# Performance work log

Hardware: AMD Instinct MI355X
Metric: run time of the kernel (lower is better)

Reference implementation:

```python
import jax, jax.numpy as jnp
import numpy as np

B, L, H, W = 16, 4096, 64, 64
SEQ = 1024  # target_sequence_length (hardcoded in the torch module)
SP = 32     # sqrt(SEQ)


def _conv1d(x, w, b, pad):
    y = jax.lax.conv_general_dilated(x, w, (1,), [(pad, pad)],
                                     dimension_numbers=('NCH', 'OIH', 'NCH'))
    return y + b[None, :, None]


def _conv2d(x, w, b, pad, groups=1):
    y = jax.lax.conv_general_dilated(x, w, (1, 1), [(pad, pad)] * 2,
                                     feature_group_count=groups,
                                     dimension_numbers=('NCHW', 'OIHW', 'NCHW'))
    return y + b[None, :, None, None]


def _forward(us_input, img_input, us_w1, us_b1, us_w2, us_b2, us_w3, us_b3,
             aff_w, aff_w_high, aff_thr, img_w1, img_b1, img_w2, img_b2, img_w3, img_b3,
             db_qkv_w, db_qkv_b, db_dw_w, db_dw_b, db_proj_w, db_proj_b,
             db_fc_w, db_fc_b, db_dep_w, db_dep_b, db_temp,
             ca_qkv_w, ca_qkv_b, ca_out_w, ca_out_b,
             tf_ch1_w, tf_ch1_b, tf_ch2_w, tf_ch2_b,
             tf_sp1_w, tf_sp1_b, tf_sp2_w, tf_sp2_b, cls_w, cls_b):
    b = us_input.shape[0]
    # ---- ultrasound 1D conv branch ----
    x = us_input.transpose(0, 2, 1)                    # [B,1,L]
    x = jax.nn.relu(_conv1d(x, us_w1, us_b1, 1))
    x = jax.nn.relu(_conv1d(x, us_w2, us_b2, 1))
    x = jax.nn.relu(_conv1d(x, us_w3, us_b3, 1))
    us_feat = x.transpose(0, 2, 1)                     # [B,L,64]
    # ---- adaptive frequency filtering (training-mode high-freq mask included) ----
    n = us_feat.shape[1]
    xf = jnp.fft.rfft(us_feat, axis=1, norm='ortho')   # [B,Nf,64] complex
    w_c = aff_w[:, 0] + 1j * aff_w[:, 1]
    xw = xf * w_c
    energy = jnp.sum(jnp.abs(xf) ** 2, axis=-1)        # [B,Nf]
    med = jnp.median(energy.reshape(b, -1), axis=1, keepdims=True)
    ne = energy / (med + 1e-6)
    hard = (ne > aff_thr).astype(jnp.float32)
    mask = jax.lax.stop_gradient(hard - aff_thr) + aff_thr  # straight-through threshold
    wh_c = aff_w_high[:, 0] + 1j * aff_w_high[:, 1]
    xw = xw + (xf * mask[..., None]) * wh_c
    us_feat = jnp.fft.irfft(xw, n=n, axis=1, norm='ortho')  # [B,L,64]
    # ---- image 2D conv branch ----
    y = jax.nn.relu(_conv2d(img_input, img_w1, img_b1, 1))
    y = jax.nn.relu(_conv2d(y, img_w2, img_b2, 1))
    y = jax.nn.relu(_conv2d(y, img_w3, img_b3, 1))     # [B,64,H,W]
    # ---- dual-branch feature fusion block ----
    hgt, wid = y.shape[2], y.shape[3]
    hw = hgt * wid
    qkv = jnp.einsum('oi,bihw->bohw', db_qkv_w, y) + db_qkv_b[None, :, None, None]
    qkv = _conv2d(qkv, db_dw_w, db_dw_b, 1, groups=192)      # depthwise (3x3x3 conv @ D=1 -> center 3x3)
    # convolutional branch: faithful row-major reshape as in torch
    f_all = qkv.reshape(b, hw, 12, 16).transpose(0, 2, 1, 3)  # [B,12,HW,16]
    f_all = jnp.einsum('oi,bink->bonk', db_fc_w, f_all) + db_fc_b[None, :, None, None]
    f_conv = f_all.transpose(0, 3, 1, 2).reshape(b, 144, hgt, wid)
    out_conv = _conv2d(f_conv, db_dep_w, db_dep_b, 1, groups=16)  # [B,64,H,W]
    # channel attention branch
    q, k, v = jnp.split(qkv, 3, axis=1)
    q = q.reshape(b, 4, 16, hw)
    k = k.reshape(b, 4, 16, hw)
    v = v.reshape(b, 4, 16, hw)
    q = q / jnp.maximum(jnp.linalg.norm(q, axis=-1, keepdims=True), 1e-12)
    k = k / jnp.maximum(jnp.linalg.norm(k, axis=-1, keepdims=True), 1e-12)
    attn = jax.nn.softmax(jnp.einsum('bhcn,bhdn->bhcd', q, k) * db_temp, axis=-1)
    out = jnp.einsum('bhcd,bhdn->bhcn', attn, v).reshape(b, 64, hgt, wid)
    out = jnp.einsum('oi,bihw->bohw', db_proj_w, out) + db_proj_b[None, :, None, None]
    img_feat = (out + out_conv).reshape(b, 64, hw).transpose(0, 2, 1)  # [B,HW,64]
    # ---- adaptive avg pool to SEQ (lengths divide evenly) ----
    us_red = us_feat.transpose(0, 2, 1).reshape(b, 64, SEQ, -1).mean(-1).transpose(0, 2, 1)
    img_red = img_feat.transpose(0, 2, 1).reshape(b, 64, SEQ, -1).mean(-1).transpose(0, 2, 1)
    # ---- cross-modal attention (shared qkv/out projections) ----
    def heads(t):
        u = (jnp.einsum('bli,oi->blo', t, ca_qkv_w) + ca_qkv_b).reshape(b, SEQ, 4, 3, 16)
        return (u[:, :, :, 0].transpose(0, 2, 1, 3),
                u[:, :, :, 1].transpose(0, 2, 1, 3),
                u[:, :, :, 2].transpose(0, 2, 1, 3))
    q1, k1, v1 = heads(us_red)
    q2, k2, v2 = heads(img_red)
    scale = 1.0 / jnp.sqrt(jnp.float32(16.0))
    a1 = jax.nn.softmax(jnp.einsum('bhqd,bhkd->bhqk', q1, k2) * scale, axis=-1)
    a2 = jax.nn.softmax(jnp.einsum('bhqd,bhkd->bhqk', q2, k1) * scale, axis=-1)
    o1 = jnp.einsum('bhqk,bhkd->bhqd', a1, v2).transpose(0, 2, 1, 3).reshape(b, SEQ, 64)
    o2 = jnp.einsum('bhqk,bhkd->bhqd', a2, v1).transpose(0, 2, 1, 3).reshape(b, SEQ, 64)
    o1 = jnp.einsum('bli,oi->blo', o1, ca_out_w) + ca_out_b
    o2 = jnp.einsum('bli,oi->blo', o2, ca_out_w) + ca_out_b
    t1 = o1.transpose(0, 2, 1).reshape(b, 64, SP, SP)
    t2 = o2.transpose(0, 2, 1).reshape(b, 64, SP, SP)
    # ---- modal fusion attention (channel + spatial gating) ----
    ch_pool = jnp.stack([t1.mean((2, 3)), t1.max((2, 3)), t2.mean((2, 3)), t2.max((2, 3))], axis=1)  # [B,4,64]
    c1 = _conv1d(ch_pool, tf_ch1_w, tf_ch1_b, 1)      # [B,1,64]
    c2 = _conv1d(ch_pool, tf_ch2_w, tf_ch2_b, 1)
    ch_stack = jax.nn.softmax(jnp.stack([c1, c2], 0), axis=0)      # [2,B,1,64]
    ch_stack = ch_stack.transpose(0, 1, 3, 2)[..., None]           # [2,B,64,1,1]
    sp_pool = jnp.concatenate([t1.mean(1, keepdims=True), t1.max(1, keepdims=True),
                               t2.mean(1, keepdims=True), t2.max(1, keepdims=True)], axis=1)
    s1 = _conv2d(sp_pool, tf_sp1_w, tf_sp1_b, 3)
    s2 = _conv2d(sp_pool, tf_sp2_w, tf_sp2_b, 3)
    sp_stack = jax.nn.softmax(jnp.stack([s1, s2], 0), axis=0)      # [2,B,1,SP,SP]
    att = ch_stack + sp_stack + 1.0                                # [2,B,64,SP,SP]
    fuse = att[0] * t1 + att[1] * t2
    logits = fuse.mean((2, 3)) @ cls_w.T + cls_b
    return jax.nn.softmax(logits, axis=1)


def setup_inputs() -> dict:
    key = jax.random.key(0)
    ks = iter(jax.random.split(key, 64))
    def rn(shape, s=0.2):
        return jax.random.normal(next(ks), shape, dtype=jnp.float32) * s
    d = {
        'us_input': jax.random.normal(next(ks), (B, L, 1), dtype=jnp.float32),
        'img_input': jax.random.normal(next(ks), (B, 3, H, W), dtype=jnp.float32),
        'us_w1': rn((16, 1, 3)), 'us_b1': rn((16,), 0.02),
        'us_w2': rn((32, 16, 3)), 'us_b2': rn((32,), 0.02),
        'us_w3': rn((64, 32, 3)), 'us_b3': rn((64,), 0.02),
        'aff_w': rn((64, 2), 0.02), 'aff_w_high': rn((64, 2), 0.02),
        'aff_thr': jax.random.uniform(next(ks), (1,), dtype=jnp.float32),
        'img_w1': rn((16, 3, 3, 3)), 'img_b1': rn((16,), 0.02),
        'img_w2': rn((32, 16, 3, 3)), 'img_b2': rn((32,), 0.02),
        'img_w3': rn((64, 32, 3, 3)), 'img_b3': rn((64,), 0.02),
        'db_qkv_w': rn((192, 64), 0.1), 'db_qkv_b': rn((192,), 0.02),
        'db_dw_w': rn((192, 1, 3, 3)), 'db_dw_b': rn((192,), 0.02),
        'db_proj_w': rn((64, 64), 0.1), 'db_proj_b': rn((64,), 0.02),
        'db_fc_w': rn((9, 12), 0.1), 'db_fc_b': rn((9,), 0.02),
        'db_dep_w': rn((64, 9, 3, 3), 0.1), 'db_dep_b': rn((64,), 0.02),
        'db_temp': jnp.ones((4, 1, 1), dtype=jnp.float32),
        'ca_qkv_w': rn((192, 64), 0.1), 'ca_qkv_b': rn((192,), 0.02),
        'ca_out_w': rn((64, 64), 0.1), 'ca_out_b': rn((64,), 0.02),
        'tf_ch1_w': rn((1, 4, 3)), 'tf_ch1_b': rn((1,), 0.02),
        'tf_ch2_w': rn((1, 4, 3)), 'tf_ch2_b': rn((1,), 0.02),
        'tf_sp1_w': rn((1, 4, 7, 7)), 'tf_sp1_b': rn((1,), 0.02),
        'tf_sp2_w': rn((1, 4, 7, 7)), 'tf_sp2_b': rn((1,), 0.02),
        'cls_w': rn((9, 64), 0.1), 'cls_b': rn((9,), 0.02),
    }
    return d


def reference(us_input, img_input, us_w1, us_b1, us_w2, us_b2, us_w3, us_b3,
              aff_w, aff_w_high, aff_thr, img_w1, img_b1, img_w2, img_b2, img_w3, img_b3,
              db_qkv_w, db_qkv_b, db_dw_w, db_dw_b, db_proj_w, db_proj_b,
              db_fc_w, db_fc_b, db_dep_w, db_dep_b, db_temp,
              ca_qkv_w, ca_qkv_b, ca_out_w, ca_out_b,
              tf_ch1_w, tf_ch1_b, tf_ch2_w, tf_ch2_b,
              tf_sp1_w, tf_sp1_b, tf_sp2_w, tf_sp2_b, cls_w, cls_b):
    return _forward(us_input, img_input, us_w1, us_b1, us_w2, us_b2, us_w3, us_b3,
                    aff_w, aff_w_high, aff_thr, img_w1, img_b1, img_w2, img_b2, img_w3, img_b3,
                    db_qkv_w, db_qkv_b, db_dw_w, db_dw_b, db_proj_w, db_proj_b,
                    db_fc_w, db_fc_b, db_dep_w, db_dep_b, db_temp,
                    ca_qkv_w, ca_qkv_b, ca_out_w, ca_out_b,
                    tf_ch1_w, tf_ch1_b, tf_ch2_w, tf_ch2_b,
                    tf_sp1_w, tf_sp1_b, tf_sp2_w, tf_sp2_b, cls_w, cls_b)
```

## Files before the change

### kernel.cpp

```cpp
#include <hip/hip_runtime.h>

typedef float v2f __attribute__((ext_vector_type(2)));

static constexpr size_t O_SMALL   = 0;
static constexpr size_t O_US3     = 3145728;
static constexpr size_t O_XF      = 7340032;
static constexpr size_t O_USFILT  = 11536384;
static constexpr size_t O_ENERGY  = 15730688;
static constexpr size_t O_MED     = 15764480;
static constexpr size_t O_NRM     = 15765504;
static constexpr size_t O_ATTNS   = 15767552;
static constexpr size_t O_CHPOOL  = 15783936;
static constexpr size_t O_CHW     = 15788032;
static constexpr size_t O_SPPOOL  = 15790080;
static constexpr size_t O_SPW     = 15855616;
static constexpr size_t O_QKV     = 15888384;
static constexpr size_t O_QKVDW   = 28471296;
static constexpr size_t O_OUTCONV = 41054208;
static constexpr size_t CA_USRED = 0, CA_IMGRED = 1, CA_Q1 = 2, CA_K1 = 3, CA_V1 = 4,
                        CA_Q2 = 5, CA_K2 = 6, CA_V2 = 7, CA_O1 = 8, CA_O2 = 9,
                        CA_T1 = 10, CA_T2 = 11;


template<int Ci, int Co>
__device__ __forceinline__ void conv1d3_body(char* smem_raw, int bid,
    const float* __restrict__ in, const float* __restrict__ w,
    const float* __restrict__ bs, float* __restrict__ out)
{
    constexpr int T = 128;
    constexpr int G = 256 / Co;
    constexpr int N = T / G;
    auto lds = (float(*)[T + 2])smem_raw;
    int tid = threadIdx.x;
    int b  = bid >> 5;
    int t0 = (bid & 31) * T;
    const float* inb = in + (size_t)b * Ci * 4096;
    for (int i = tid; i < Ci * T; i += 256) {
        int ci = i / T, x = i % T;
        lds[ci][x + 1] = inb[ci * 4096 + t0 + x];
    }
    if (tid < Ci) {
        lds[tid][0]     = (t0 > 0)        ? inb[tid * 4096 + t0 - 1] : 0.f;
        lds[tid][T + 1] = (t0 + T < 4096) ? inb[tid * 4096 + t0 + T] : 0.f;
    }
    __syncthreads();
    int co = tid / G;
    int x0 = (tid % G) * N;
    float acc[N];
    float bias = bs[co];
#pragma unroll
    for (int j = 0; j < N; ++j) acc[j] = bias;
    const float* wb = w + co * Ci * 3;
    for (int ci = 0; ci < Ci; ++ci) {
        float w0 = wb[ci * 3], w1 = wb[ci * 3 + 1], w2 = wb[ci * 3 + 2];
        float a = lds[ci][x0], bb = lds[ci][x0 + 1];
#pragma unroll
        for (int j = 0; j < N; ++j) {
            float cc = lds[ci][x0 + 2 + j];
            acc[j] += w0 * a + w1 * bb + w2 * cc;
            a = bb; bb = cc;
        }
    }
    float* ob = out + ((size_t)b * Co + co) * 4096 + t0 + x0;
#pragma unroll
    for (int j = 0; j < N; ++j) ob[j] = fmaxf(acc[j], 0.f);
}

template<int Ci, int Co, int TY>
__device__ __forceinline__ void conv2d3_body(char* smem_raw, int bid,
    const float* __restrict__ in, const float* __restrict__ w,
    const float* __restrict__ bs, float* __restrict__ out)
{
    constexpr int G = 256 / (Co * TY);
    constexpr int N = 64 / G;
    auto lds = (float(*)[TY + 2][66])smem_raw;
    int tid = threadIdx.x;
    constexpr int NB = 64 / TY;
    int b  = bid / NB;
    int y0 = (bid % NB) * TY;
    const float* inb = in + (size_t)b * Ci * 4096;
    for (int i = tid; i < Ci * (TY + 2) * 64; i += 256) {
        int x  = i & 63;
        int ry = (i >> 6) % (TY + 2);
        int ci = i / ((TY + 2) * 64);
        int gy = y0 - 1 + ry;
        lds[ci][ry][x + 1] = (gy >= 0 && gy < 64) ? inb[ci * 4096 + gy * 64 + x] : 0.f;
    }
    for (int r = tid; r < Ci * (TY + 2); r += 256) {
        int ry = r % (TY + 2), ci = r / (TY + 2);
        lds[ci][ry][0] = 0.f; lds[ci][ry][65] = 0.f;
    }
    __syncthreads();
    int co   = tid / (TY * G);
    int ysub = (tid / G) % TY;
    int x0   = (tid % G) * N;
    float acc[N];
    float bias = bs[co];
#pragma unroll
    for (int j = 0; j < N; ++j) acc[j] = bias;
    const float* wb = w + co * Ci * 9;
    for (int ci = 0; ci < Ci; ++ci) {
        float wr[9];
#pragma unroll
        for (int k = 0; k < 9; ++k) wr[k] = wb[ci * 9 + k];
#pragma unroll
        for (int dy = 0; dy < 3; ++dy) {
            const float* lr = &lds[ci][ysub + dy][x0];
            float a = lr[0], bb = lr[1];
#pragma unroll
            for (int j = 0; j < N; ++j) {
                float cc = lr[2 + j];
                acc[j] += wr[dy * 3] * a + wr[dy * 3 + 1] * bb + wr[dy * 3 + 2] * cc;
                a = bb; bb = cc;
            }
        }
    }
    float* ob = out + ((size_t)b * Co + co) * 4096 + (y0 + ysub) * 64 + x0;
#pragma unroll
    for (int j = 0; j < N; ++j) ob[j] = fmaxf(acc[j], 0.f);
}

__device__ __forceinline__ void fft4096_r4(float2* A, float2* B, int tid)
{
    float2* src = A; float2* dst = B;
    int Ns = 1;
    for (int s = 0; s < 6; ++s) {
        float cfac = -0.25f / (float)Ns;
        for (int r = 0; r < 4; ++r) {
            int j = (r << 8) + tid;
            float2 v0 = src[j];
            float2 v1 = src[j + 1024];
            float2 v2 = src[j + 2048];
            float2 v3 = src[j + 3072];
            int jm = j & (Ns - 1);
            float rev = (float)jm * cfac;
            float s1 = __builtin_amdgcn_sinf(rev);
            float c1 = __builtin_amdgcn_cosf(rev);
            float c2 = c1 * c1 - s1 * s1, s2 = 2.f * c1 * s1;
            float c3 = c2 * c1 - s2 * s1, s3 = c2 * s1 + s2 * c1;
            float2 u1 = make_float2(v1.x * c1 - v1.y * s1, v1.x * s1 + v1.y * c1);
            float2 u2 = make_float2(v2.x * c2 - v2.y * s2, v2.x * s2 + v2.y * c2);
            float2 u3 = make_float2(v3.x * c3 - v3.y * s3, v3.x * s3 + v3.y * c3);
            float t0x = v0.x + u2.x, t0y = v0.y + u2.y;
            float t1x = v0.x - u2.x, t1y = v0.y - u2.y;
            float t2x = u1.x + u3.x, t2y = u1.y + u3.y;
            float t3x = u1.x - u3.x, t3y = u1.y - u3.y;
            int base = ((j - jm) << 2) + jm;
            dst[base]          = make_float2(t0x + t2x, t0y + t2y);
            dst[base + Ns]     = make_float2(t1x + t3y, t1y - t3x);
            dst[base + 2 * Ns] = make_float2(t0x - t2x, t0y - t2y);
            dst[base + 3 * Ns] = make_float2(t1x - t3y, t1y + t3x);
        }
        __syncthreads();
        float2* tmp = src; src = dst; dst = tmp;
        Ns <<= 2;
    }
}

__device__ __forceinline__ void fft_fwd_body(char* smem_raw, int row,
    const float* __restrict__ us3, float* __restrict__ xf)
{
    float2* A  = (float2*)smem_raw;
    float2* Bb = A + 4096;
    int tid = threadIdx.x;
    const float* x = us3 + (size_t)row * 4096;
    for (int r = 0; r < 16; ++r) {
        int i = (r << 8) + tid;
        A[i] = make_float2(x[i], 0.f);
    }
    __syncthreads();
    fft4096_r4(A, Bb, tid);
    float* out = xf + (size_t)row * 4098;
    for (int r = 0; r < 9; ++r) {
        int f = (r << 8) + tid;
        if (f < 2049) {
            out[2 * f]     = A[f].x * (1.f / 64.f);
            out[2 * f + 1] = A[f].y * (1.f / 64.f);
        }
    }
}

__device__ __forceinline__ void energy_body(int bid,
    const float* __restrict__ xf, float* __restrict__ energy)
{
    int idx = bid * 256 + threadIdx.x;
    if (idx >= 16 * 2049) return;
    int b = idx / 2049, f = idx % 2049;
    const float* p = xf + (size_t)b * 64 * 4098 + 2 * f;
    float e = 0.f;
    for (int ch = 0; ch < 64; ++ch) {
        float re = p[0], im = p[1];
        e += re * re + im * im;
        p += 4098;
    }
    energy[idx] = e;
}

__device__ __forceinline__ void median_body(char* smem_raw, int b,
    const float* __restrict__ energy, float* __restrict__ med)
{
    float* s = (float*)smem_raw;
    int tid = threadIdx.x;
    for (int r = 0; r < 16; ++r) {
        int i = (r << 8) + tid;
        s[i] = (i < 2049) ? energy[b * 2049 + i] : 3.0e38f;
    }
    __syncthreads();
    for (int k = 2; k <= 4096; k <<= 1) {
        for (int j = k >> 1; j > 0; j >>= 1) {
            for (int r = 0; r < 16; ++r) {
                int i = (r << 8) + tid;
                int ixj = i ^ j;
                if (ixj > i) {
                    bool up = ((i & k) == 0);
                    float a = s[i], bb = s[ixj];
                    if ((a > bb) == up) { s[i] = bb; s[ixj] = a; }
                }
            }
            __syncthreads();
        }
    }
    if (tid == 0) med[b] = s[1024];
}

__device__ __forceinline__ void filter_ifft_body(char* smem_raw, int row,
    const float* __restrict__ xf, const float* __restrict__ energy,
    const float* __restrict__ med, const float* __restrict__ aff_w,
    const float* __restrict__ aff_wh, const float* __restrict__ thr_p,
    float* __restrict__ us_filt)
{
    float2* A  = (float2*)smem_raw;
    float2* Bb = A + 4096;
    int b = row >> 6, ch = row & 63;
    int tid = threadIdx.x;
    float thr = thr_p[0];
    float mden = med[b] + 1e-6f;
    float w0r = aff_w[2 * ch], w0i = aff_w[2 * ch + 1];
    float whr = aff_wh[2 * ch], whi = aff_wh[2 * ch + 1];
    const float* X = xf + (size_t)row * 4098;
    const float* E = energy + b * 2049;
    for (int r = 0; r < 9; ++r) {
        int f = (r << 8) + tid;
        if (f < 2049) {
            float re = X[2 * f], im = X[2 * f + 1];
            float mask = (E[f] / mden > thr) ? 1.f : 0.f;
            float wr = w0r + mask * whr;
            float wi = w0i + mask * whi;
            float xr = re * wr - im * wi;
            float xi = re * wi + im * wr;
            A[f] = make_float2(xr, -xi);
            if (f >= 1 && f <= 2047) A[4096 - f] = make_float2(xr, xi);
        }
    }
    __syncthreads();
    fft4096_r4(A, Bb, tid);
    float* out = us_filt + (size_t)row * 4096;
    for (int r = 0; r < 16; ++r) {
        int i = (r << 8) + tid;
        out[i] = A[i].x * (1.f / 64.f);
    }
}

__device__ __forceinline__ void qkv1x1_body(int bid, const float* __restrict__ y,
    const float* __restrict__ w, const float* __restrict__ bs, float* __restrict__ out)
{
    int oc = bid & 3;
    int pc = (bid >> 2) & 15;
    int b  = bid >> 6;
    int p = pc * 256 + threadIdx.x;
    const float* inb = y + (size_t)b * 262144 + p;
    v2f reg[32];
#pragma unroll
    for (int ci = 0; ci < 32; ++ci) {
        v2f r; r.x = inb[(2 * ci) * 4096]; r.y = inb[(2 * ci + 1) * 4096];
        reg[ci] = r;
    }
    float* ob = out + (size_t)b * 786432 + (size_t)oc * 48 * 4096 + p;
    for (int o = 0; o < 48; ++o) {
        const v2f* wr = (const v2f*)(w + (oc * 48 + o) * 64);
        v2f s2 = {0.f, 0.f};
#pragma unroll
        for (int ci = 0; ci < 32; ++ci) s2 = wr[ci] * reg[ci] + s2;
        ob[o * 4096] = bs[oc * 48 + o] + s2.x + s2.y;
    }
}

__device__ __forceinline__ void dwconv_body(int bid, const float* __restrict__ in,
    const float* __restrict__ w, const float* __restrict__ bs, float* __restrict__ out)
{
    int idx = bid * 256 + threadIdx.x;
    int x = idx & 63, yy = (idx >> 6) & 63;
    int c = (idx >> 12) % 192;
    const float* p = in + idx;
    const float* wp = w + c * 9;
    float acc = bs[c];
    bool ym = yy > 0, yp = yy < 63, xm = x > 0, xp = x < 63;
    float s = wp[4] * p[0];
    if (ym) { s += wp[1] * p[-64]; if (xm) s += wp[0] * p[-65]; if (xp) s += wp[2] * p[-63]; }
    if (xm) s += wp[3] * p[-1];
    if (xp) s += wp[5] * p[1];
    if (yp) { s += wp[7] * p[64];  if (xm) s += wp[6] * p[63];  if (xp) s += wp[8] * p[65]; }
    out[idx] = acc + s;
}

__device__ __forceinline__ void fc_body(int bid, const float* __restrict__ qkv_dw,
    const float* __restrict__ fw, const float* __restrict__ fb, float* __restrict__ fcv)
{
    int idx = bid * 256 + threadIdx.x;
    int k = idx & 15;
    int p = (idx >> 4) & 4095;
    int b = idx >> 16;
    const float* base = qkv_dw + (size_t)b * 786432;
    float u[12];
#pragma unroll
    for (int i = 0; i < 12; ++i) u[i] = base[p * 192 + i * 16 + k];
#pragma unroll
    for (int o = 0; o < 9; ++o) {
        float s = fb[o];
#pragma unroll
        for (int i = 0; i < 12; ++i) s += fw[o * 12 + i] * u[i];
        fcv[(((size_t)b * 16 + k) * 9 + o) * 4096 + p] = s;
    }
}

__device__ __forceinline__ void depconv2_body(char* smem_raw, int bid,
    const float* __restrict__ fcv, const float* __restrict__ w,
    const float* __restrict__ bs, float* __restrict__ out)
{
    auto lds = (float(*)[10][66])smem_raw;
    int band = bid & 7;
    int g    = (bid >> 3) & 15;
    int b    = bid >> 7;
    int y0 = band * 8;
    int tid = threadIdx.x;
    const float* inb = fcv + ((size_t)(b * 16 + g) * 9) * 4096;
    for (int i = tid; i < 9 * 10 * 64; i += 256) {
        int x  = i & 63;
        int ry = (i >> 6) % 10;
        int ci = i / 640;
        int gy = y0 - 1 + ry;
        lds[ci][ry][x + 1] = (gy >= 0 && gy < 64) ? inb[ci * 4096 + gy * 64 + x] : 0.f;
    }
    for (int i = tid; i < 90; i += 256) {
        int ry = i % 10, ci = i / 10;
        lds[ci][ry][0] = 0.f; lds[ci][ry][65] = 0.f;
    }
    __syncthreads();
    int co   = tid >> 6;
    int ysub = (tid >> 3) & 7;
    int x0   = (tid & 7) * 8;
    int ocg  = g * 4 + co;
    float acc[8];
    float bias = bs[ocg];
#pragma unroll
    for (int j = 0; j < 8; ++j) acc[j] = bias;
    const float* wb = w + ocg * 81;
    for (int ci = 0; ci < 9; ++ci) {
        float wr[9];
#pragma unroll
        for (int k = 0; k < 9; ++k) wr[k] = wb[ci * 9 + k];
#pragma unroll
        for (int dy = 0; dy < 3; ++dy) {
            const float* lr = &lds[ci][ysub + dy][x0];
            float a = lr[0], bb = lr[1];
#pragma unroll
            for (int j = 0; j < 8; ++j) {
                float cc = lr[2 + j];
                acc[j] += wr[dy * 3] * a + wr[dy * 3 + 1] * bb + wr[dy * 3 + 2] * cc;
                a = bb; bb = cc;
            }
        }
    }
    float* ob = out + ((size_t)b * 64 + ocg) * 4096 + (y0 + ysub) * 64 + x0;
#pragma unroll
    for (int j = 0; j < 8; ++j) ob[j] = acc[j];
}

__device__ __forceinline__ void qknorm_body(char* smem_raw, int row,
    const float* __restrict__ qkv_dw, float* __restrict__ nrm)
{
    float* red = (float*)smem_raw;
    int which = row >> 10;
    int r = row & 1023;
    int b = r >> 6, hd = r & 63;
    const float* p = qkv_dw + ((size_t)b * 192 + which * 64 + hd) * 4096;
    float s = 0.f;
    for (int i = threadIdx.x; i < 4096; i += 256) { float v = p[i]; s += v * v; }
    red[threadIdx.x] = s;
    __syncthreads();
    for (int st = 128; st > 0; st >>= 1) {
        if (threadIdx.x < st) red[threadIdx.x] += red[threadIdx.x + st];
        __syncthreads();
    }
    if (threadIdx.x == 0) nrm[row] = sqrtf(red[0]);
}

__device__ __forceinline__ void chpool2_body(int bid, const float* __restrict__ t1,
    const float* __restrict__ t2, float* __restrict__ chpool)
{
    int rg = bid & 15;
    int b  = bid >> 4;
    int wave = threadIdx.x >> 6, lane = threadIdx.x & 63;
    int c = rg * 4 + wave;
    const float* p1 = t1 + ((size_t)b * 64 + c) * 1024;
    const float* p2 = t2 + ((size_t)b * 64 + c) * 1024;
    float m1 = 0.f, x1 = -3e38f, m2 = 0.f, x2 = -3e38f;
#pragma unroll
    for (int i = 0; i < 16; ++i) {
        int p = lane + i * 64;
        float a = p1[p], bb = p2[p];
        m1 += a; x1 = fmaxf(x1, a);
        m2 += bb; x2 = fmaxf(x2, bb);
    }
    for (int off = 32; off > 0; off >>= 1) {
        m1 += __shfl_xor(m1, off);
        x1 = fmaxf(x1, __shfl_xor(x1, off));
        m2 += __shfl_xor(m2, off);
        x2 = fmaxf(x2, __shfl_xor(x2, off));
    }
    if (lane == 0) {
        chpool[b * 256 + c]       = m1 * (1.f / 1024.f);
        chpool[b * 256 + 64 + c]  = x1;
        chpool[b * 256 + 128 + c] = m2 * (1.f / 1024.f);
        chpool[b * 256 + 192 + c] = x2;
    }
}

__device__ __forceinline__ void sppool_body(int bid, const float* __restrict__ t1,
    const float* __restrict__ t2, float* __restrict__ sppool)
{
    int b = bid >> 2;
    int p = (bid & 3) * 256 + threadIdx.x;
    float m1 = 0.f, x1 = -3e38f, m2 = 0.f, x2 = -3e38f;
    const float* p1 = t1 + (size_t)b * 65536 + p;
    const float* p2 = t2 + (size_t)b * 65536 + p;
    for (int c = 0; c < 64; ++c) {
        float a = p1[c * 1024], bb = p2[c * 1024];
        m1 += a; x1 = fmaxf(x1, a);
        m2 += bb; x2 = fmaxf(x2, bb);
    }
    sppool[b * 4096 + p]        = m1 * (1.f / 64.f);
    sppool[b * 4096 + 1024 + p] = x1;
    sppool[b * 4096 + 2048 + p] = m2 * (1.f / 64.f);
    sppool[b * 4096 + 3072 + p] = x2;
}

__device__ __forceinline__ void chgate_body(int b, const float* __restrict__ chpool,
    const float* __restrict__ w1, const float* __restrict__ b1,
    const float* __restrict__ w2, const float* __restrict__ b2, float* __restrict__ chw)
{
    int c = threadIdx.x;
    if (c >= 64) return;
    float a1 = b1[0], a2 = b2[0];
    for (int ic = 0; ic < 4; ++ic) {
        const float* cp = chpool + b * 256 + ic * 64;
        for (int d = -1; d <= 1; ++d) {
            int cc = c + d;
            if (cc >= 0 && cc < 64) {
                a1 += w1[ic * 3 + d + 1] * cp[cc];
                a2 += w2[ic * 3 + d + 1] * cp[cc];
            }
        }
    }
    float mx = fmaxf(a1, a2);
    float e1 = __expf(a1 - mx), e2 = __expf(a2 - mx);
    float inv = 1.f / (e1 + e2);
    chw[b * 64 + c]        = e1 * inv;
    chw[1024 + b * 64 + c] = e2 * inv;
}

__device__ __forceinline__ void spgate_body(int bid, const float* __restrict__ sppool,
    const float* __restrict__ w1, const float* __restrict__ b1,
    const float* __restrict__ w2, const float* __restrict__ b2, float* __restrict__ spw)
{
    int idx = bid * 256 + threadIdx.x;
    int p = idx & 1023;
    int b = idx >> 10;
    int y = p >> 5, x = p & 31;
    float a1 = b1[0], a2 = b2[0];
    for (int ic = 0; ic < 4; ++ic) {
        const float* sp = sppool + b * 4096 + ic * 1024;
        for (int dy = -3; dy <= 3; ++dy) {
            int yy = y + dy;
            if (yy < 0 || yy > 31) continue;
            for (int dx = -3; dx <= 3; ++dx) {
                int xx = x + dx;
                if (xx < 0 || xx > 31) continue;
                float v = sp[yy * 32 + xx];
                int wi = ic * 49 + (dy + 3) * 7 + (dx + 3);
                a1 += w1[wi] * v;
                a2 += w2[wi] * v;
            }
        }
    }
    float mx = fmaxf(a1, a2);
    float e1 = __expf(a1 - mx), e2 = __expf(a2 - mx);
    float inv = 1.f / (e1 + e2);
    spw[idx]         = e1 * inv;
    spw[16384 + idx] = e2 * inv;
}


__global__ __launch_bounds__(256) void s1_kernel(const float* us_in, const float* uw, const float* ub,
    float* uo, const float* iin, const float* iw, const float* ib, float* io)
{
    __shared__ __align__(16) char smem[3168];
    if (blockIdx.x < 512) conv1d3_body<1, 16>(smem, blockIdx.x, us_in, uw, ub, uo);
    else                  conv2d3_body<3, 16, 2>(smem, blockIdx.x - 512, iin, iw, ib, io);
}

__global__ __launch_bounds__(256) void s2_kernel(const float* ui, const float* uw, const float* ub,
    float* uo, const float* ii, const float* iw, const float* ib, float* io)
{
    __shared__ __align__(16) char smem[16896];
    if (blockIdx.x < 512) conv1d3_body<16, 32>(smem, blockIdx.x, ui, uw, ub, uo);
    else                  conv2d3_body<16, 32, 2>(smem, blockIdx.x - 512, ii, iw, ib, io);
}

__global__ __launch_bounds__(256) void s3_kernel(const float* ui, const float* uw, const float* ub,
    float* uo, const float* ii, const float* iw, const float* ib, float* io)
{
    __shared__ __align__(16) char smem[33792];
    if (blockIdx.x < 512) conv1d3_body<32, 64>(smem, blockIdx.x, ui, uw, ub, uo);
    else                  conv2d3_body<32, 64, 2>(smem, blockIdx.x - 512, ii, iw, ib, io);
}

__global__ __launch_bounds__(256) void s4_kernel(const float* us3, float* xf,
    const float* y, const float* qw, const float* qb, float* qkv)
{
    __shared__ __align__(16) char smem[65536];
    if (blockIdx.x < 1024) fft_fwd_body(smem, blockIdx.x, us3, xf);
    else                   qkv1x1_body(blockIdx.x - 1024, y, qw, qb, qkv);
}

__global__ __launch_bounds__(256) void s5_kernel(const float* qkv, const float* dww,
    const float* dwb, float* qkv_dw, const float* xf, float* energy)
{
    if (blockIdx.x < 49152) dwconv_body(blockIdx.x, qkv, dww, dwb, qkv_dw);
    else                    energy_body(blockIdx.x - 49152, xf, energy);
}

__global__ __launch_bounds__(256) void s6_kernel(const float* qkv_dw, const float* fw,
    const float* fb, float* fcv, const float* energy, float* med)
{
    __shared__ __align__(16) char smem[16384];
    if (blockIdx.x < 4096) fc_body(blockIdx.x, qkv_dw, fw, fb, fcv);
    else                   median_body(smem, blockIdx.x - 4096, energy, med);
}

__global__ __launch_bounds__(256) void s7_kernel(const float* fcv, const float* dw,
    const float* db, float* out_conv, const float* qkv_dw, float* nrm,
    const float* xf, const float* energy, const float* med, const float* aw,
    const float* awh, const float* thr, float* us_filt)
{
    __shared__ __align__(16) char smem[65536];
    if (blockIdx.x < 2048)      depconv2_body(smem, blockIdx.x, fcv, dw, db, out_conv);
    else if (blockIdx.x < 4096) qknorm_body(smem, blockIdx.x - 2048, qkv_dw, nrm);
    else                        filter_ifft_body(smem, blockIdx.x - 4096, xf, energy, med, aw, awh, thr, us_filt);
}

__global__ __launch_bounds__(256) void s16_kernel(const float* t1, const float* t2,
    float* chpool, float* sppool)
{
    if (blockIdx.x < 256) chpool2_body(blockIdx.x, t1, t2, chpool);
    else                  sppool_body(blockIdx.x - 256, t1, t2, sppool);
}

__global__ __launch_bounds__(256) void s17_kernel(const float* sppool, const float* sw1,
    const float* sb1, const float* sw2, const float* sb2, float* spw,
    const float* chpool, const float* cw1, const float* cb1, const float* cw2,
    const float* cb2, float* chw)
{
    if (blockIdx.x < 64) spgate_body(blockIdx.x, sppool, sw1, sb1, sw2, sb2, spw);
    else                 chgate_body(blockIdx.x - 64, chpool, cw1, cb1, cw2, cb2, chw);
}


__global__ __launch_bounds__(256) void chan_attn_kernel(
    const float* __restrict__ qkv_dw, const float* __restrict__ nrm,
    const float* __restrict__ temp, float* __restrict__ attn_s)
{
    int bh = blockIdx.x;
    int b = bh >> 2, h = bh & 3;
    __shared__ float Qs[16][130];
    __shared__ float Ks2[16][130];
    int c = threadIdx.x >> 4, d = threadIdx.x & 15;
    const float* qbase = qkv_dw + ((size_t)b * 192 + h * 16) * 4096;
    const float* kbase = qkv_dw + ((size_t)b * 192 + 64 + h * 16) * 4096;
    float s = 0.f;
    for (int n0 = 0; n0 < 4096; n0 += 128) {
        __syncthreads();
        for (int r = 0; r < 8; ++r) {
            int i = (r << 8) + threadIdx.x;
            int row = i >> 7, col = i & 127;
            Qs[row][col]  = qbase[(size_t)row * 4096 + n0 + col];
            Ks2[row][col] = kbase[(size_t)row * 4096 + n0 + col];
        }
        __syncthreads();
#pragma unroll 8
        for (int n = 0; n < 128; ++n) s += Qs[c][n] * Ks2[d][n];
    }
    float nq = fmaxf(nrm[b * 64 + h * 16 + c], 1e-12f);
    float nk = fmaxf(nrm[1024 + b * 64 + h * 16 + d], 1e-12f);
    s = s / (nq * nk) * temp[h];
    __shared__ float S[16][17];
    S[c][d] = s;
    __syncthreads();
    if (threadIdx.x < 16) {
        int cc = threadIdx.x;
        float mx = -3e30f;
        for (int dd = 0; dd < 16; ++dd) mx = fmaxf(mx, S[cc][dd]);
        float sm = 0.f;
        float e[16];
        for (int dd = 0; dd < 16; ++dd) { e[dd] = __expf(S[cc][dd] - mx); sm += e[dd]; }
        float inv = 1.f / sm;
        float* dst = attn_s + (size_t)bh * 256 + cc * 16;
        for (int dd = 0; dd < 16; ++dd) dst[dd] = e[dd] * inv;
    }
}

__global__ __launch_bounds__(256, 2) void attnproj_kernel(const float* __restrict__ attn_s,
    const float* __restrict__ qkv_dw, const float* __restrict__ outconv,
    const float* __restrict__ pw, const float* __restrict__ pb, float* __restrict__ img_feat)
{
    int blk = blockIdx.x;
    int oc = blk & 1;
    int pc = (blk >> 1) & 15;
    int b  = blk >> 5;
    int n = pc * 256 + threadIdx.x;
    const float* vb = qkv_dw + ((size_t)b * 192 + 128) * 4096 + n;
    v2f v[32];
#pragma unroll
    for (int i = 0; i < 32; ++i) {
        v2f r; r.x = vb[(2 * i) * 4096]; r.y = vb[(2 * i + 1) * 4096];
        v[i] = r;
    }
    const float* ab = attn_s + (size_t)b * 1024;
    for (int h = 0; h < 4; ++h) {
        v2f tmp[8];
#pragma unroll
        for (int c2 = 0; c2 < 8; ++c2) {
            v2f s2a = {0.f, 0.f}, s2b = {0.f, 0.f};
            const v2f* r0 = (const v2f*)(ab + (h * 16 + 2 * c2) * 16);
            const v2f* r1 = (const v2f*)(ab + (h * 16 + 2 * c2 + 1) * 16);
#pragma unroll
            for (int d2 = 0; d2 < 8; ++d2) {
                s2a = r0[d2] * v[h * 8 + d2] + s2a;
                s2b = r1[d2] * v[h * 8 + d2] + s2b;
            }
            v2f t; t.x = s2a.x + s2a.y; t.y = s2b.x + s2b.y;
            tmp[c2] = t;
        }
#pragma unroll
        for (int c2 = 0; c2 < 8; ++c2) v[h * 8 + c2] = tmp[c2];
    }
    float* ofb = img_feat + (size_t)b * 262144 + (size_t)oc * 32 * 4096 + n;
    const float* ocb = outconv + (size_t)b * 262144 + (size_t)oc * 32 * 4096 + n;
    for (int o = 0; o < 32; ++o) {
        const v2f* wr = (const v2f*)(pw + (oc * 32 + o) * 64);
        v2f s2 = {0.f, 0.f};
#pragma unroll
        for (int c2 = 0; c2 < 32; ++c2) s2 = wr[c2] * v[c2] + s2;
        ofb[o * 4096] = pb[oc * 32 + o] + ocb[o * 4096] + s2.x + s2.y;
    }
}

__global__ __launch_bounds__(256) void poolred_kernel(const float* __restrict__ us_filt,
    const float* __restrict__ img_feat, float* __restrict__ us_redT, float* __restrict__ img_redT)
{
    int idx = blockIdx.x * 256 + threadIdx.x;
    int s4 = idx & 1023;
    int c = (idx >> 10) & 63;
    int b = (idx >> 16) & 15;
    int m = idx >> 20;
    const float* in = (m ? img_feat : us_filt) + ((size_t)b * 64 + c) * 4096 + s4 * 4;
    float4 v4 = *(const float4*)in;
    float v = 0.25f * (v4.x + v4.y + v4.z + v4.w);
    (m ? img_redT : us_redT)[((size_t)b * 64 + c) * 1024 + s4] = v;
}

__global__ __launch_bounds__(256, 2) void caqkv2_kernel(const float* __restrict__ us_redT,
    const float* __restrict__ img_redT, const float* __restrict__ qw, const float* __restrict__ qb,
    float* __restrict__ q1, float* __restrict__ k1, float* __restrict__ v1,
    float* __restrict__ q2, float* __restrict__ k2, float* __restrict__ v2)
{
    int blk = blockIdx.x;
    int h  = blk & 3;
    int pc = (blk >> 2) & 3;
    int b  = (blk >> 4) & 15;
    int m  = blk >> 8;
    int l = pc * 256 + threadIdx.x;
    const float* in = (m ? img_redT : us_redT) + (size_t)b * 65536 + l;
    v2f reg[32];
#pragma unroll
    for (int i = 0; i < 32; ++i) {
        v2f r; r.x = in[(2 * i) * 1024]; r.y = in[(2 * i + 1) * 1024];
        reg[i] = r;
    }
    size_t rowoff = ((size_t)(b * 4 + h) * 1024 + l) * 16;
    float* dst[3] = { (m ? q2 : q1) + rowoff, (m ? k2 : k1) + rowoff, (m ? v2 : v1) + rowoff };
#pragma unroll
    for (int which = 0; which < 3; ++which) {
        float* dp = dst[which];
        for (int d = 0; d < 16; ++d) {
            int o = h * 48 + which * 16 + d;
            const v2f* wr = (const v2f*)(qw + o * 64);
            v2f s2 = {0.f, 0.f};
#pragma unroll
            for (int i = 0; i < 32; ++i) s2 = wr[i] * reg[i] + s2;
            dp[d] = qb[o] + s2.x + s2.y;
        }
    }
}

__global__ __launch_bounds__(256) void kmax_kernel(const float* __restrict__ k1,
    const float* __restrict__ k2, float* __restrict__ kmax)
{
    int unit = blockIdx.x;
    int h = unit & 3, m = (unit >> 2) & 1, b = unit >> 3;
    const float* K = m ? k1 : k2;
    const float* Kb = K + (size_t)(b * 4 + h) * 16384;
    int tid = threadIdx.x;
    float mx = 0.f;
#pragma unroll
    for (int j = 0; j < 4; ++j) {
        const float* kp = Kb + (size_t)(tid + 256 * j) * 16;
        float s = 0.f;
#pragma unroll
        for (int d = 0; d < 16; ++d) s += kp[d] * kp[d];
        mx = fmaxf(mx, s);
    }
    for (int off = 32; off > 0; off >>= 1) mx = fmaxf(mx, __shfl_xor(mx, off));
    __shared__ float red[4];
    if ((tid & 63) == 0) red[tid >> 6] = mx;
    __syncthreads();
    if (tid == 0) {
        float r = fmaxf(fmaxf(red[0], red[1]), fmaxf(red[2], red[3]));
        kmax[unit] = sqrtf(r);
    }
}

__global__ __launch_bounds__(256, 2) void cross_attn6_kernel(
    const float* __restrict__ q1, const float* __restrict__ k1, const float* __restrict__ v1,
    const float* __restrict__ q2, const float* __restrict__ k2, const float* __restrict__ v2,
    const float* __restrict__ kmax, float* __restrict__ ls_, float* __restrict__ accp)
{
    int blk  = blockIdx.x;
    int kt   = blk & 3;
    int unit = blk >> 2;
    int h = unit & 3;
    int m = (unit >> 2) & 1;
    int b = unit >> 3;
    const float* Q = m ? q2 : q1;
    const float* K = m ? k1 : k2;
    const float* V = m ? v1 : v2;
    const float* Qb = Q + (size_t)(b * 4 + h) * 16384;
    const float* Kb = K + (size_t)(b * 4 + h) * 16384 + kt * 256 * 16;
    const float* Vb = V + (size_t)(b * 4 + h) * 16384 + kt * 256 * 16;
    int tid = threadIdx.x;
    const float SC = 0.25f * 1.44269504088896340736f;
    float km = kmax[unit];
    v2f qr[4][8], acc[4][8];
    float M[4], ls[4];
#pragma unroll
    for (int j = 0; j < 4; ++j) {
        const v2f* qp = (const v2f*)(Qb + (size_t)(tid + 256 * j) * 16);
        v2f qs2 = {0.f, 0.f};
#pragma unroll
        for (int i = 0; i < 8; ++i) {
            v2f q = qp[i];
            qs2 = q * q + qs2;
            qr[j][i] = q * SC;
        }
        M[j] = sqrtf(qs2.x + qs2.y) * km * SC;
        ls[j] = 0.f;
#pragma unroll
        for (int i = 0; i < 8; ++i) acc[j][i] = (v2f){0.f, 0.f};
    }
    __shared__ float Ks[64 * 16];
    __shared__ float Vs[64 * 16];
    for (int t0 = 0; t0 < 256; t0 += 64) {
        __syncthreads();
        ((float4*)Ks)[tid] = ((const float4*)(Kb + t0 * 16))[tid];
        ((float4*)Vs)[tid] = ((const float4*)(Vb + t0 * 16))[tid];
        __syncthreads();
#pragma unroll 2
        for (int t = 0; t < 64; ++t) {
            const v2f* k2p = (const v2f*)&Ks[t * 16];
            v2f kk[8];
#pragma unroll
            for (int i = 0; i < 8; ++i) kk[i] = k2p[i];
            float p[4];
#pragma unroll
            for (int j = 0; j < 4; ++j) {
                v2f s2 = {0.f, 0.f};
#pragma unroll
                for (int i = 0; i < 8; ++i) s2 = qr[j][i] * kk[i] + s2;
                p[j] = exp2f(s2.x + s2.y - M[j]);
                ls[j] += p[j];
            }
            const v2f* v2p = (const v2f*)&Vs[t * 16];
            v2f vv[8];
#pragma unroll
            for (int i = 0; i < 8; ++i) vv[i] = v2p[i];
#pragma unroll
            for (int j = 0; j < 4; ++j) {
                v2f pj = {p[j], p[j]};
#pragma unroll
                for (int i = 0; i < 8; ++i) acc[j][i] = pj * vv[i] + acc[j][i];
            }
        }
    }
#pragma unroll
    for (int j = 0; j < 4; ++j) {
        int q = tid + 256 * j;
        size_t pi = (size_t)(unit * 4 + kt) * 1024 + q;
        ls_[pi] = ls[j];
        v2f* ap = (v2f*)(accp + pi * 16);
#pragma unroll
        for (int i = 0; i < 8; ++i) ap[i] = acc[j][i];
    }
}

__global__ __launch_bounds__(256) void ca_merge2_kernel(const float* __restrict__ ls_,
    const float* __restrict__ accp, float* __restrict__ o1t, float* __restrict__ o2t)
{
    int idx = blockIdx.x * 256 + threadIdx.x;
    int q = idx & 1023;
    int unit = idx >> 10;
    int h = unit & 3;
    int m = (unit >> 2) & 1;
    int b = unit >> 3;
    float l = 0.f;
#pragma unroll
    for (int i = 0; i < 4; ++i) l += ls_[(size_t)(unit * 4 + i) * 1024 + q];
    float inv = 1.f / l;
    float* dst = (m ? o2t : o1t) + (size_t)b * 65536 + (size_t)(h * 16) * 1024 + q;
#pragma unroll
    for (int d = 0; d < 16; ++d) {
        float s = 0.f;
#pragma unroll
        for (int i = 0; i < 4; ++i) s += accp[((size_t)(unit * 4 + i) * 1024 + q) * 16 + d];
        dst[d * 1024] = s * inv;
    }
}

__global__ __launch_bounds__(256, 2) void caout2_kernel(const float* __restrict__ o1t,
    const float* __restrict__ o2t, const float* __restrict__ ow, const float* __restrict__ ob_,
    float* __restrict__ t1, float* __restrict__ t2)
{
    int blk = blockIdx.x;
    int oc = blk & 1;
    int pc = (blk >> 1) & 3;
    int b  = (blk >> 3) & 15;
    int m  = blk >> 7;
    int l = pc * 256 + threadIdx.x;
    const float* in = (m ? o2t : o1t) + (size_t)b * 65536 + l;
    v2f reg[32];
#pragma unroll
    for (int i = 0; i < 32; ++i) {
        v2f r; r.x = in[(2 * i) * 1024]; r.y = in[(2 * i + 1) * 1024];
        reg[i] = r;
    }
    float* t = (m ? t2 : t1) + (size_t)b * 65536 + (size_t)oc * 32 * 1024 + l;
    for (int o = 0; o < 32; ++o) {
        const v2f* wr = (const v2f*)(ow + (oc * 32 + o) * 64);
        v2f s2 = {0.f, 0.f};
#pragma unroll
        for (int i = 0; i < 32; ++i) s2 = wr[i] * reg[i] + s2;
        t[o * 1024] = ob_[oc * 32 + o] + s2.x + s2.y;
    }
}

__global__ __launch_bounds__(256) void final2_kernel(const float* __restrict__ t1,
    const float* __restrict__ t2, const float* __restrict__ chw, const float* __restrict__ spw,
    const float* __restrict__ clsw, const float* __restrict__ clsb, float* __restrict__ out)
{
    int b = blockIdx.x;
    int wave = threadIdx.x >> 6, lane = threadIdx.x & 63;
    __shared__ float feat[64];
    __shared__ float lg[9];
    const float* s1 = spw + b * 1024;
    const float* s2 = spw + 16384 + b * 1024;
    for (int round = 0; round < 16; ++round) {
        int c = round * 4 + wave;
        float g1 = chw[b * 64 + c] + 1.f;
        float g2 = chw[1024 + b * 64 + c] + 1.f;
        const float* p1 = t1 + ((size_t)b * 64 + c) * 1024;
        const float* p2 = t2 + ((size_t)b * 64 + c) * 1024;
        float acc = 0.f;
#pragma unroll
        for (int i = 0; i < 16; ++i) {
            int p = lane + i * 64;
            acc += (g1 + s1[p]) * p1[p] + (g2 + s2[p]) * p2[p];
        }
        for (int off = 32; off > 0; off >>= 1) acc += __shfl_xor(acc, off);
        if (lane == 0) feat[c] = acc * (1.f / 1024.f);
    }
    __syncthreads();
    if (threadIdx.x < 9) {
        int c = threadIdx.x;
        float s = clsb[c];
        for (int i = 0; i < 64; ++i) s += clsw[c * 64 + i] * feat[i];
        lg[c] = s;
    }
    __syncthreads();
    if (threadIdx.x == 0) {
        float mx = -3e38f;
        for (int o = 0; o < 9; ++o) mx = fmaxf(mx, lg[o]);
        float sm = 0.f;
        float e[9];
        for (int o = 0; o < 9; ++o) { e[o] = __expf(lg[o] - mx); sm += e[o]; }
        float inv = 1.f / sm;
        for (int o = 0; o < 9; ++o) out[b * 9 + o] = e[o] * inv;
    }
}

extern "C" void kernel_launch(void* const* d_in, const int* in_sizes, int n_in,
                              void* d_out, int out_size, void* d_ws, size_t ws_size,
                              hipStream_t stream)
{
    (void)in_sizes; (void)n_in; (void)out_size; (void)ws_size;
    const float* us_input = (const float*)d_in[0];
    const float* img_input = (const float*)d_in[1];
    const float* us_w1 = (const float*)d_in[2];  const float* us_b1 = (const float*)d_in[3];
    const float* us_w2 = (const float*)d_in[4];  const float* us_b2 = (const float*)d_in[5];
    const float* us_w3 = (const float*)d_in[6];  const float* us_b3 = (const float*)d_in[7];
    const float* aff_w = (const float*)d_in[8];  const float* aff_wh = (const float*)d_in[9];
    const float* aff_thr = (const float*)d_in[10];
    const float* img_w1 = (const float*)d_in[11]; const float* img_b1 = (const float*)d_in[12];
    const float* img_w2 = (const float*)d_in[13]; const float* img_b2 = (const float*)d_in[14];
    const float* img_w3 = (const float*)d_in[15]; const float* img_b3 = (const float*)d_in[16];
    const float* db_qkv_w = (const float*)d_in[17]; const float* db_qkv_b = (const float*)d_in[18];
    const float* db_dw_w = (const float*)d_in[19];  const float* db_dw_b = (const float*)d_in[20];
    const float* db_proj_w = (const float*)d_in[21]; const float* db_proj_b = (const float*)d_in[22];
    const float* db_fc_w = (const float*)d_in[23];  const float* db_fc_b = (const float*)d_in[24];
    const float* db_dep_w = (const float*)d_in[25]; const float* db_dep_b = (const float*)d_in[26];
    const float* db_temp = (const float*)d_in[27];
    const float* ca_qkv_w = (const float*)d_in[28]; const float* ca_qkv_b = (const float*)d_in[29];
    const float* ca_out_w = (const float*)d_in[30]; const float* ca_out_b = (const float*)d_in[31];
    const float* tf_ch1_w = (const float*)d_in[32]; const float* tf_ch1_b = (const float*)d_in[33];
    const float* tf_ch2_w = (const float*)d_in[34]; const float* tf_ch2_b = (const float*)d_in[35];
    const float* tf_sp1_w = (const float*)d_in[36]; const float* tf_sp1_b = (const float*)d_in[37];
    const float* tf_sp2_w = (const float*)d_in[38]; const float* tf_sp2_b = (const float*)d_in[39];
    const float* cls_w = (const float*)d_in[40];   const float* cls_b = (const float*)d_in[41];

    float* ws = (float*)d_ws;
    float* us1     = ws + O_SMALL;
    float* us2     = ws + O_SMALL + 1048576;
    float* us3     = ws + O_US3;
    float* xf      = ws + O_XF;
    float* us_filt = ws + O_USFILT;
    float* energy  = ws + O_ENERGY;
    float* med     = ws + O_MED;
    float* nrm     = ws + O_NRM;
    float* attn_s  = ws + O_ATTNS;
    float* chpool  = ws + O_CHPOOL;
    float* chw     = ws + O_CHW;
    float* sppool  = ws + O_SPPOOL;
    float* spw     = ws + O_SPW;
    float* qkv     = ws + O_QKV;
    float* qkv_dw  = ws + O_QKVDW;
    float* out_conv= ws + O_OUTCONV;
    float* img1 = ws + O_USFILT;
    float* img2 = ws + O_USFILT + 1048576;
    float* y = ws + O_QKVDW;
    float* fcv = qkv;
    float* img_feat = xf;
    float* us_redT  = ws + O_QKV + CA_USRED  * 1048576;
    float* img_redT = ws + O_QKV + CA_IMGRED * 1048576;
    float* q1 = ws + O_QKV + CA_Q1 * 1048576;
    float* k1 = ws + O_QKV + CA_K1 * 1048576;
    float* v1 = ws + O_QKV + CA_V1 * 1048576;
    float* q2 = ws + O_QKV + CA_Q2 * 1048576;
    float* k2 = ws + O_QKV + CA_K2 * 1048576;
    float* v2 = ws + O_QKV + CA_V2 * 1048576;
    float* o1t = ws + O_QKV + CA_O1 * 1048576;
    float* o2t = ws + O_QKV + CA_O2 * 1048576;
    float* t1 = ws + O_QKV + CA_T1 * 1048576;
    float* t2 = ws + O_QKV + CA_T2 * 1048576;
    float* ca_accp = ws + O_QKVDW;
    float* ca_ls   = ws + O_QKVDW + 8388608;
    float* ca_kmax = ws + O_QKVDW + 8912896;

    s1_kernel<<<1024, 256, 0, stream>>>(us_input, us_w1, us_b1, us1,
                                        img_input, img_w1, img_b1, img1);
    s2_kernel<<<1024, 256, 0, stream>>>(us1, us_w2, us_b2, us2,
                                        img1, img_w2, img_b2, img2);
    s3_kernel<<<1024, 256, 0, stream>>>(us2, us_w3, us_b3, us3,
                                        img2, img_w3, img_b3, y);
    s4_kernel<<<2048, 256, 0, stream>>>(us3, xf, y, db_qkv_w, db_qkv_b, qkv);
    s5_kernel<<<49281, 256, 0, stream>>>(qkv, db_dw_w, db_dw_b, qkv_dw, xf, energy);
    s6_kernel<<<4112, 256, 0, stream>>>(qkv_dw, db_fc_w, db_fc_b, fcv, energy, med);
    s7_kernel<<<5120, 256, 0, stream>>>(fcv, db_dep_w, db_dep_b, out_conv,
                                        qkv_dw, nrm, xf, energy, med,
                                        aff_w, aff_wh, aff_thr, us_filt);
    chan_attn_kernel<<<64, 256, 0, stream>>>(qkv_dw, nrm, db_temp, attn_s);
    attnproj_kernel<<<512, 256, 0, stream>>>(attn_s, qkv_dw, out_conv, db_proj_w, db_proj_b, img_feat);
    poolred_kernel<<<8192, 256, 0, stream>>>(us_filt, img_feat, us_redT, img_redT);
    caqkv2_kernel<<<512, 256, 0, stream>>>(us_redT, img_redT, ca_qkv_w, ca_qkv_b,
                                           q1, k1, v1, q2, k2, v2);
    kmax_kernel<<<128, 256, 0, stream>>>(k1, k2, ca_kmax);
    cross_attn6_kernel<<<512, 256, 0, stream>>>(q1, k1, v1, q2, k2, v2, ca_kmax, ca_ls, ca_accp);
    ca_merge2_kernel<<<512, 256, 0, stream>>>(ca_ls, ca_accp, o1t, o2t);
    caout2_kernel<<<256, 256, 0, stream>>>(o1t, o2t, ca_out_w, ca_out_b, t1, t2);
    s16_kernel<<<320, 256, 0, stream>>>(t1, t2, chpool, sppool);
    s17_kernel<<<80, 256, 0, stream>>>(sppool, tf_sp1_w, tf_sp1_b, tf_sp2_w, tf_sp2_b, spw,
                                       chpool, tf_ch1_w, tf_ch1_b, tf_ch2_w, tf_ch2_b, chw);
    final2_kernel<<<16, 256, 0, stream>>>(t1, t2, chw, spw, cls_w, cls_b, (float*)d_out);
}
```

Baseline: 988.0 us.

## Split s7 by shared-memory needs, split-K channel attention, drop LDS staging in cross-attn

```diff
diff --git a/kernel.cpp b/kernel.cpp
--- a/kernel.cpp
+++ b/kernel.cpp
@@ -548,15 +548,19 @@
     else                   median_body(smem, blockIdx.x - 4096, energy, med);
 }
 
-__global__ __launch_bounds__(256) void s7_kernel(const float* fcv, const float* dw,
-    const float* db, float* out_conv, const float* qkv_dw, float* nrm,
-    const float* xf, const float* energy, const float* med, const float* aw,
-    const float* awh, const float* thr, float* us_filt)
+__global__ __launch_bounds__(256) void s7a_kernel(const float* fcv, const float* dw,
+    const float* db, float* out_conv, const float* qkv_dw, float* nrm)
+{
+    __shared__ __align__(16) char smem[23808];
+    if (blockIdx.x < 2048) depconv2_body(smem, blockIdx.x, fcv, dw, db, out_conv);
+    else                   qknorm_body(smem, blockIdx.x - 2048, qkv_dw, nrm);
+}
+
+__global__ __launch_bounds__(256) void filt_kernel(const float* xf, const float* energy,
+    const float* med, const float* aw, const float* awh, const float* thr, float* us_filt)
 {
     __shared__ __align__(16) char smem[65536];
-    if (blockIdx.x < 2048)      depconv2_body(smem, blockIdx.x, fcv, dw, db, out_conv);
-    else if (blockIdx.x < 4096) qknorm_body(smem, blockIdx.x - 2048, qkv_dw, nrm);
-    else                        filter_ifft_body(smem, blockIdx.x - 4096, xf, energy, med, aw, awh, thr, us_filt);
+    filter_ifft_body(smem, blockIdx.x, xf, energy, med, aw, awh, thr, us_filt);
 }
 
 __global__ __launch_bounds__(256) void s16_kernel(const float* t1, const float* t2,
@@ -576,19 +580,20 @@
 }
 
 
-__global__ __launch_bounds__(256) void chan_attn_kernel(
-    const float* __restrict__ qkv_dw, const float* __restrict__ nrm,
-    const float* __restrict__ temp, float* __restrict__ attn_s)
-{
-    int bh = blockIdx.x;
+__global__ __launch_bounds__(256) void chan_attn_part_kernel(
+    const float* __restrict__ qkv_dw, float* __restrict__ part)
+{
+    int blk = blockIdx.x;
+    int nc = blk & 7;
+    int bh = blk >> 3;
     int b = bh >> 2, h = bh & 3;
     __shared__ float Qs[16][130];
     __shared__ float Ks2[16][130];
     int c = threadIdx.x >> 4, d = threadIdx.x & 15;
-    const float* qbase = qkv_dw + ((size_t)b * 192 + h * 16) * 4096;
-    const float* kbase = qkv_dw + ((size_t)b * 192 + 64 + h * 16) * 4096;
+    const float* qbase = qkv_dw + ((size_t)b * 192 + h * 16) * 4096 + nc * 512;
+    const float* kbase = qkv_dw + ((size_t)b * 192 + 64 + h * 16) * 4096 + nc * 512;
     float s = 0.f;
-    for (int n0 = 0; n0 < 4096; n0 += 128) {
+    for (int n0 = 0; n0 < 512; n0 += 128) {
         __syncthreads();
         for (int r = 0; r < 8; ++r) {
             int i = (r << 8) + threadIdx.x;
@@ -600,6 +605,19 @@
 #pragma unroll 8
         for (int n = 0; n < 128; ++n) s += Qs[c][n] * Ks2[d][n];
     }
+    part[(size_t)blk * 256 + threadIdx.x] = s;
+}
+
+__global__ __launch_bounds__(256) void chan_attn_merge_kernel(
+    const float* __restrict__ part, const float* __restrict__ nrm,
+    const float* __restrict__ temp, float* __restrict__ attn_s)
+{
+    int bh = blockIdx.x;
+    int b = bh >> 2, h = bh & 3;
+    int c = threadIdx.x >> 4, d = threadIdx.x & 15;
+    float s = 0.f;
+#pragma unroll
+    for (int i = 0; i < 8; ++i) s += part[(size_t)(bh * 8 + i) * 256 + threadIdx.x];
     float nq = fmaxf(nrm[b * 64 + h * 16 + c], 1e-12f);
     float nk = fmaxf(nrm[1024 + b * 64 + h * 16 + d], 1e-12f);
     s = s / (nq * nk) * temp[h];
@@ -619,6 +637,7 @@
     }
 }
 
+
 __global__ __launch_bounds__(256, 2) void attnproj_kernel(const float* __restrict__ attn_s,
     const float* __restrict__ qkv_dw, const float* __restrict__ outconv,
     const float* __restrict__ pw, const float* __restrict__ pb, float* __restrict__ img_feat)
@@ -740,7 +759,7 @@
     }
 }
 
-__global__ __launch_bounds__(256, 2) void cross_attn6_kernel(
+__global__ __launch_bounds__(256, 2) void cross_attn7_kernel(
     const float* __restrict__ q1, const float* __restrict__ k1, const float* __restrict__ v1,
     const float* __restrict__ q2, const float* __restrict__ k2, const float* __restrict__ v2,
     const float* __restrict__ kmax, float* __restrict__ ls_, float* __restrict__ accp)
@@ -777,38 +796,30 @@
 #pragma unroll
         for (int i = 0; i < 8; ++i) acc[j][i] = (v2f){0.f, 0.f};
     }
-    __shared__ float Ks[64 * 16];
-    __shared__ float Vs[64 * 16];
-    for (int t0 = 0; t0 < 256; t0 += 64) {
-        __syncthreads();
-        ((float4*)Ks)[tid] = ((const float4*)(Kb + t0 * 16))[tid];
-        ((float4*)Vs)[tid] = ((const float4*)(Vb + t0 * 16))[tid];
-        __syncthreads();
 #pragma unroll 2
-        for (int t = 0; t < 64; ++t) {
-            const v2f* k2p = (const v2f*)&Ks[t * 16];
-            v2f kk[8];
-#pragma unroll
-            for (int i = 0; i < 8; ++i) kk[i] = k2p[i];
-            float p[4];
-#pragma unroll
-            for (int j = 0; j < 4; ++j) {
-                v2f s2 = {0.f, 0.f};
-#pragma unroll
-                for (int i = 0; i < 8; ++i) s2 = qr[j][i] * kk[i] + s2;
-                p[j] = exp2f(s2.x + s2.y - M[j]);
-                ls[j] += p[j];
-            }
-            const v2f* v2p = (const v2f*)&Vs[t * 16];
-            v2f vv[8];
-#pragma unroll
-            for (int i = 0; i < 8; ++i) vv[i] = v2p[i];
-#pragma unroll
-            for (int j = 0; j < 4; ++j) {
-                v2f pj = {p[j], p[j]};
-#pragma unroll
-                for (int i = 0; i < 8; ++i) acc[j][i] = pj * vv[i] + acc[j][i];
-            }
+    for (int t = 0; t < 256; ++t) {
+        const v2f* kp = (const v2f*)(Kb + t * 16);
+        v2f kk[8];
+#pragma unroll
+        for (int i = 0; i < 8; ++i) kk[i] = kp[i];
+        float p[4];
+#pragma unroll
+        for (int j = 0; j < 4; ++j) {
+            v2f s2 = {0.f, 0.f};
+#pragma unroll
+            for (int i = 0; i < 8; ++i) s2 = qr[j][i] * kk[i] + s2;
+            p[j] = exp2f(s2.x + s2.y - M[j]);
+            ls[j] += p[j];
+        }
+        const v2f* vp = (const v2f*)(Vb + t * 16);
+        v2f vv[8];
+#pragma unroll
+        for (int i = 0; i < 8; ++i) vv[i] = vp[i];
+#pragma unroll
+        for (int j = 0; j < 4; ++j) {
+            v2f pj = {p[j], p[j]};
+#pragma unroll
+            for (int i = 0; i < 8; ++i) acc[j][i] = pj * vv[i] + acc[j][i];
         }
     }
 #pragma unroll
@@ -967,6 +978,7 @@
     float* y = ws + O_QKVDW;
     float* fcv = qkv;
     float* img_feat = xf;
+    float* ca_part = ws + O_XF + 3000000;
     float* us_redT  = ws + O_QKV + CA_USRED  * 1048576;
     float* img_redT = ws + O_QKV + CA_IMGRED * 1048576;
     float* q1 = ws + O_QKV + CA_Q1 * 1048576;
@@ -992,16 +1004,16 @@
     s4_kernel<<<2048, 256, 0, stream>>>(us3, xf, y, db_qkv_w, db_qkv_b, qkv);
     s5_kernel<<<49281, 256, 0, stream>>>(qkv, db_dw_w, db_dw_b, qkv_dw, xf, energy);
     s6_kernel<<<4112, 256, 0, stream>>>(qkv_dw, db_fc_w, db_fc_b, fcv, energy, med);
-    s7_kernel<<<5120, 256, 0, stream>>>(fcv, db_dep_w, db_dep_b, out_conv,
-                                        qkv_dw, nrm, xf, energy, med,
-                                        aff_w, aff_wh, aff_thr, us_filt);
-    chan_attn_kernel<<<64, 256, 0, stream>>>(qkv_dw, nrm, db_temp, attn_s);
+    s7a_kernel<<<4096, 256, 0, stream>>>(fcv, db_dep_w, db_dep_b, out_conv, qkv_dw, nrm);
+    filt_kernel<<<1024, 256, 0, stream>>>(xf, energy, med, aff_w, aff_wh, aff_thr, us_filt);
+    chan_attn_part_kernel<<<512, 256, 0, stream>>>(qkv_dw, ca_part);
+    chan_attn_merge_kernel<<<64, 256, 0, stream>>>(ca_part, nrm, db_temp, attn_s);
     attnproj_kernel<<<512, 256, 0, stream>>>(attn_s, qkv_dw, out_conv, db_proj_w, db_proj_b, img_feat);
     poolred_kernel<<<8192, 256, 0, stream>>>(us_filt, img_feat, us_redT, img_redT);
     caqkv2_kernel<<<512, 256, 0, stream>>>(us_redT, img_redT, ca_qkv_w, ca_qkv_b,
                                            q1, k1, v1, q2, k2, v2);
     kmax_kernel<<<128, 256, 0, stream>>>(k1, k2, ca_kmax);
-    cross_attn6_kernel<<<512, 256, 0, stream>>>(q1, k1, v1, q2, k2, v2, ca_kmax, ca_ls, ca_accp);
+    cross_attn7_kernel<<<512, 256, 0, stream>>>(q1, k1, v1, q2, k2, v2, ca_kmax, ca_ls, ca_accp);
     ca_merge2_kernel<<<512, 256, 0, stream>>>(ca_ls, ca_accp, o1t, o2t);
     caout2_kernel<<<256, 256, 0, stream>>>(o1t, o2t, ca_out_w, ca_out_b, t1, t2);
     s16_kernel<<<320, 256, 0, stream>>>(t1, t2, chpool, sppool);
```

Result: faster. 930.9 us (-5.8%).
